# Optimization experiments

Hardware: AMD Instinct MI355X
Metric: run time of the kernel (lower is better)

The kernel has to match this reference:

```python
import jax, jax.numpy as jnp
import numpy as np

C_S = 128
C_T = 128
C_OUT = 128


def _proj(x, W, b):
    # 1x1x1 Conv3d == per-voxel linear over channel dim. x: [B, Cin, T, H, W]
    return jnp.einsum('oc,bcthw->bothw', W, x) + b[None, :, None, None, None]


def setup_inputs() -> dict:
    key = jax.random.key(0)
    ks = jax.random.split(key, 12)
    B, T, H, W = 4, 4, 32, 32
    spatial_features = jax.random.normal(ks[0], (B, T, C_S, H, W), dtype=jnp.float32)
    temporal_features = jax.random.normal(ks[1], (B, C_T, T, H, W), dtype=jnp.float32)
    def w(k, o, i):
        return jax.random.normal(k, (o, i), dtype=jnp.float32) * (i ** -0.5)
    return {
        'spatial_features': spatial_features,
        'temporal_features': temporal_features,
        'Wq': w(ks[2], C_OUT, C_S), 'bq': jnp.zeros((C_OUT,), jnp.float32),
        'Wk': w(ks[3], C_OUT, C_T), 'bk': jnp.zeros((C_OUT,), jnp.float32),
        'Wv': w(ks[4], C_OUT, C_T), 'bv': jnp.zeros((C_OUT,), jnp.float32),
        'Wo': w(ks[5], C_OUT, C_OUT), 'bo': jnp.zeros((C_OUT,), jnp.float32),
    }


def reference(spatial_features, temporal_features, Wq, bq, Wk, bk, Wv, bv, Wo, bo):
    B, T, C_s, H, W = spatial_features.shape
    N = T * H * W
    scale = C_OUT ** -0.5
    # permute(0,2,1,3,4): [B, T, C_s, H, W] -> [B, C_s, T, H, W]
    x_s = jnp.transpose(spatial_features, (0, 2, 1, 3, 4))
    q = _proj(x_s, Wq, bq)                 # [B, C_out, T, H, W]
    k = _proj(temporal_features, Wk, bk)   # [B, C_out, T, H, W]
    v = _proj(temporal_features, Wv, bv)   # [B, C_out, T, H, W]
    Q = q.reshape(B, C_OUT, N).transpose(0, 2, 1)  # [B, N, C]
    K = k.reshape(B, C_OUT, N)                     # [B, C, N]
    V = v.reshape(B, C_OUT, N).transpose(0, 2, 1)  # [B, N, C]
    attn = jax.nn.softmax(jnp.einsum('bnc,bcm->bnm', Q, K) * scale, axis=2)  # [B, N, N]
    out = jnp.einsum('bnm,bmc->bnc', attn, V)      # [B, N, C]
    out = out.transpose(0, 2, 1).reshape(B, C_OUT, T, H, W)
    return _proj(out, Wo, bo)
```

## Files before the change

### kernel.cpp

```cpp
#include <hip/hip_runtime.h>
#include <cstddef>

#define NDIM 4096
#define SCALE 0.08838834764831843f
#define SOFT_BIAS 8.0f

typedef _Float16 h8 __attribute__((ext_vector_type(8)));
typedef _Float16 h4 __attribute__((ext_vector_type(4)));
typedef _Float16 h2 __attribute__((ext_vector_type(2)));
typedef float    f4 __attribute__((ext_vector_type(4)));

__global__ __launch_bounds__(256) void prep_w_kernel(
    const float* __restrict__ Wq, const float* __restrict__ Wk,
    const float* __restrict__ Wv, const float* __restrict__ Wo,
    _Float16* __restrict__ Wh)
{
    const int idx = (blockIdx.x * 256 + threadIdx.x) * 8;
    const int sel = idx >> 14;
    const float* src = sel == 0 ? Wq : sel == 1 ? Wk : sel == 2 ? Wv : Wo;
    const int off = idx & 16383;
    const float4 a = *(const float4*)(src + off);
    const float4 c = *(const float4*)(src + off + 4);
    h8 r;
    r[0]=(_Float16)a.x; r[1]=(_Float16)a.y; r[2]=(_Float16)a.z; r[3]=(_Float16)a.w;
    r[4]=(_Float16)c.x; r[5]=(_Float16)c.y; r[6]=(_Float16)c.z; r[7]=(_Float16)c.w;
    *(h8*)(Wh + idx) = r;
}

__global__ __launch_bounds__(256, 1) void proj_qkv_kernel(
    const float* __restrict__ spatial, const float* __restrict__ temporal,
    const _Float16* __restrict__ Wh,
    const float* __restrict__ bq, const float* __restrict__ bk,
    const float* __restrict__ bv,
    _Float16* __restrict__ Qh, _Float16* __restrict__ Kh, _Float16* __restrict__ Vt)
{
    __shared__ __align__(16) _Float16 Xs[64 * 152];
    __shared__ __align__(16) _Float16 Xt[64 * 152];
    const int tid = threadIdx.x;
    const int n0  = blockIdx.x * 64;
    const int b   = blockIdx.y;
    const int t   = n0 >> 10, hw0 = n0 & 1023;

    #pragma unroll
    for (int i = 0; i < 8; ++i) {
        const int ii = tid + 256 * i;
        const int c = ii >> 4, j = ii & 15;
        const float4 v = *(const float4*)(spatial + (((size_t)(b * 4 + t) * 128 + c) << 10)
                                          + hw0 + 4 * j);
        Xs[(4 * j + 0) * 152 + c] = (_Float16)v.x;
        Xs[(4 * j + 1) * 152 + c] = (_Float16)v.y;
        Xs[(4 * j + 2) * 152 + c] = (_Float16)v.z;
        Xs[(4 * j + 3) * 152 + c] = (_Float16)v.w;
    }
    #pragma unroll
    for (int i = 0; i < 8; ++i) {
        const int ii = tid + 256 * i;
        const int c = ii >> 4, j = ii & 15;
        const float4 v = *(const float4*)(temporal + (((size_t)(b * 128 + c)) << 12)
                                          + n0 + 4 * j);
        Xt[(4 * j + 0) * 152 + c] = (_Float16)v.x;
        Xt[(4 * j + 1) * 152 + c] = (_Float16)v.y;
        Xt[(4 * j + 2) * 152 + c] = (_Float16)v.z;
        Xt[(4 * j + 3) * 152 + c] = (_Float16)v.w;
    }
    __syncthreads();

    const int w = tid >> 6, n16 = tid & 15, q4 = (tid >> 4) & 3;
    const _Float16* __restrict__ Whq = Wh;
    const _Float16* __restrict__ Whk = Wh + 16384;
    const _Float16* __restrict__ Whv = Wh + 32768;

    h8 xs_f[4], xt_f[4];
    #pragma unroll
    for (int ks = 0; ks < 4; ++ks) {
        xs_f[ks] = *(const h8*)&Xs[(16 * w + n16) * 152 + 32 * ks + 8 * q4];
        xt_f[ks] = *(const h8*)&Xt[(16 * w + n16) * 152 + 32 * ks + 8 * q4];
    }

    {
        f4 acc[8];
        #pragma unroll
        for (int ot = 0; ot < 8; ++ot) acc[ot] = (f4)0.0f;
        #pragma unroll
        for (int ot = 0; ot < 8; ++ot)
            #pragma unroll
            for (int ks = 0; ks < 4; ++ks) {
                const h8 af = *(const h8*)(Whq + (16 * ot + n16) * 128 + 32 * ks + 8 * q4);
                acc[ot] = __builtin_amdgcn_mfma_f32_16x16x32_f16(af, xs_f[ks], acc[ot], 0, 0, 0);
            }
        #pragma unroll
        for (int ot = 0; ot < 8; ++ot) {
            const float4 bb = *(const float4*)&bq[16 * ot + 4 * q4];
            h4 r;
            r[0]=(_Float16)(acc[ot][0]+bb.x); r[1]=(_Float16)(acc[ot][1]+bb.y);
            r[2]=(_Float16)(acc[ot][2]+bb.z); r[3]=(_Float16)(acc[ot][3]+bb.w);
            *(h4*)(Qh + ((size_t)b * NDIM + n0 + 16 * w + n16) * 128 + 16 * ot + 4 * q4) = r;
        }
    }
    {
        f4 acc[8];
        #pragma unroll
        for (int ot = 0; ot < 8; ++ot) acc[ot] = (f4)0.0f;
        #pragma unroll
        for (int ot = 0; ot < 8; ++ot)
            #pragma unroll
            for (int ks = 0; ks < 4; ++ks) {
                const h8 af = *(const h8*)(Whk + (16 * ot + n16) * 128 + 32 * ks + 8 * q4);
                acc[ot] = __builtin_amdgcn_mfma_f32_16x16x32_f16(af, xt_f[ks], acc[ot], 0, 0, 0);
            }
        #pragma unroll
        for (int ot = 0; ot < 8; ++ot) {
            const float4 bb = *(const float4*)&bk[16 * ot + 4 * q4];
            h4 r;
            r[0]=(_Float16)(acc[ot][0]+bb.x); r[1]=(_Float16)(acc[ot][1]+bb.y);
            r[2]=(_Float16)(acc[ot][2]+bb.z); r[3]=(_Float16)(acc[ot][3]+bb.w);
            *(h4*)(Kh + ((size_t)b * NDIM + n0 + 16 * w + n16) * 128 + 16 * ot + 4 * q4) = r;
        }
    }
    {
        f4 acc[8];
        #pragma unroll
        for (int ct = 0; ct < 8; ++ct) acc[ct] = (f4)0.0f;
        #pragma unroll
        for (int ct = 0; ct < 8; ++ct)
            #pragma unroll
            for (int ks = 0; ks < 4; ++ks) {
                const h8 bf = *(const h8*)(Whv + (16 * ct + n16) * 128 + 32 * ks + 8 * q4);
                acc[ct] = __builtin_amdgcn_mfma_f32_16x16x32_f16(xt_f[ks], bf, acc[ct], 0, 0, 0);
            }
        #pragma unroll
        for (int ct = 0; ct < 8; ++ct) {
            const float bb = bv[16 * ct + n16];
            h4 r;
            r[0]=(_Float16)(acc[ct][0]+bb); r[1]=(_Float16)(acc[ct][1]+bb);
            r[2]=(_Float16)(acc[ct][2]+bb); r[3]=(_Float16)(acc[ct][3]+bb);
            *(h4*)(Vt + ((size_t)(b * 128 + 16 * ct + n16) << 12) + n0 + 16 * w + 4 * q4) = r;
        }
    }
}

__global__ __launch_bounds__(256, 2) void attn_kernel(
    const _Float16* __restrict__ Qh, const _Float16* __restrict__ Kh,
    const _Float16* __restrict__ Vt, _Float16* __restrict__ Opart,
    float* __restrict__ lpart)
{
    __shared__ __align__(16) _Float16 sh[14592];
    __shared__ float lred[2][2][32];
    _Float16* __restrict__ Kt = sh;
    _Float16* __restrict__ Vl = sh + 4352;
    _Float16* __restrict__ Pa = sh + 9472;

    const int tid  = threadIdx.x;
    const int w    = tid >> 6, lane = tid & 63;
    const int g    = w >> 1,  p    = w & 1;
    const int n16  = lane & 15, q4 = lane >> 4;
    const int b    = blockIdx.z, hf = blockIdx.y;
    const int n0   = blockIdx.x * 128;
    const int mb   = hf * 1024;

    _Float16* __restrict__ Pg = Pa + g * (64 * 40);

    h8 qf[4][4];
    {
        const _Float16* Qb = Qh + ((size_t)b * NDIM + n0 + 64 * g + n16) * 128;
        #pragma unroll
        for (int qs = 0; qs < 4; ++qs)
            #pragma unroll
            for (int ks = 0; ks < 4; ++ks)
                qf[qs][ks] = *(const h8*)(Qb + (size_t)(16 * qs) * 128 + 32 * ks + 8 * q4);
    }

    const int km  = tid >> 4, kc8 = (tid & 15) * 8;
    const int vc  = tid >> 2, vm8 = (tid & 3) * 8;
    const _Float16* kp = Kh + ((size_t)b * NDIM + mb + km) * 128 + kc8;
    const _Float16* vp = Vt + (((size_t)(b * 128 + vc)) << 12) + mb + vm8;
    int4 kreg0 = *(const int4*)kp;
    int4 kreg1 = *(const int4*)(kp + (size_t)16 * 128);
    int4 vreg0 = *(const int4*)vp;
    int4 vreg1 = *(const int4*)(vp + ((size_t)64 << 12));

    f4 oacc[4][4];
    #pragma unroll
    for (int i = 0; i < 4; ++i)
        #pragma unroll
        for (int j = 0; j < 4; ++j) oacc[i][j] = (f4)0.0f;
    float lsum[4] = {0.0f, 0.0f, 0.0f, 0.0f};

    for (int it = 0; it < 32; ++it) {
        __syncthreads();
        *(int4*)&Kt[km * 136 + kc8]        = kreg0;
        *(int4*)&Kt[(16 + km) * 136 + kc8] = kreg1;
        *(int4*)&Vl[vc * 40 + vm8]         = vreg0;
        *(int4*)&Vl[(64 + vc) * 40 + vm8]  = vreg1;
        __syncthreads();

        if (it < 31) {
            kp += 32 * 128; vp += 32;
            kreg0 = *(const int4*)kp;
            kreg1 = *(const int4*)(kp + (size_t)16 * 128);
            vreg0 = *(const int4*)vp;
            vreg1 = *(const int4*)(vp + ((size_t)64 << 12));
        }

        f4 sacc[4];
        #pragma unroll
        for (int qs = 0; qs < 4; ++qs) sacc[qs] = (f4)0.0f;
        #pragma unroll
        for (int ks = 0; ks < 4; ++ks) {
            const h8 kf = *(const h8*)&Kt[(16 * p + n16) * 136 + 32 * ks + 8 * q4];
            #pragma unroll
            for (int qs = 0; qs < 4; ++qs)
                sacc[qs] = __builtin_amdgcn_mfma_f32_16x16x32_f16(kf, qf[qs][ks], sacc[qs], 0, 0, 0);
        }

        #pragma unroll
        for (int qs = 0; qs < 4; ++qs) {
            h4 pk;
            #pragma unroll
            for (int r = 0; r < 4; ++r) {
                const float e = __expf(fmaf(sacc[qs][r], SCALE, -SOFT_BIAS));
                lsum[qs] += e;
                pk[r] = (_Float16)e;
            }
            *(h4*)&Pg[(16 * qs + n16) * 40 + 16 * p + 4 * q4] = pk;
        }
        __syncthreads();

        h8 pf[4], vf[4];
        #pragma unroll
        for (int qs = 0; qs < 4; ++qs)
            pf[qs] = *(const h8*)&Pg[(16 * qs + n16) * 40 + 8 * q4];
        #pragma unroll
        for (int ct = 0; ct < 4; ++ct)
            vf[ct] = *(const h8*)&Vl[(64 * p + 16 * ct + n16) * 40 + 8 * q4];
        #pragma unroll
        for (int qs = 0; qs < 4; ++qs)
            #pragma unroll
            for (int ct = 0; ct < 4; ++ct)
                oacc[qs][ct] = __builtin_amdgcn_mfma_f32_16x16x32_f16(pf[qs], vf[ct], oacc[qs][ct], 0, 0, 0);
    }

    #pragma unroll
    for (int qs = 0; qs < 4; ++qs) {
        lsum[qs] += __shfl_xor(lsum[qs], 16, 64);
        lsum[qs] += __shfl_xor(lsum[qs], 32, 64);
    }
    __syncthreads();
    if (q4 == 0) {
        #pragma unroll
        for (int qs = 0; qs < 4; ++qs) lred[g][p][0] = lred[g][p][0];
        #pragma unroll
        for (int qs = 0; qs < 2; ++qs) {
            lred[g][p][16 * qs + n16]      = lsum[qs];
        }
    }
    __syncthreads();
    if (q4 == 0) {
        float* lb = lpart + (size_t)(hf * 4 + b) * NDIM + n0 + 64 * g;
        if (p == 0) {
            #pragma unroll
            for (int qs = 0; qs < 2; ++qs)
                lb[16 * qs + n16] = lred[g][0][16 * qs + n16] + lred[g][1][16 * qs + n16];
        }
    }
    __syncthreads();
    if (q4 == 0) {
        #pragma unroll
        for (int qs = 2; qs < 4; ++qs)
            lred[g][p][16 * (qs - 2) + n16] = lsum[qs];
    }
    __syncthreads();
    if (q4 == 0 && p == 0) {
        float* lb = lpart + (size_t)(hf * 4 + b) * NDIM + n0 + 64 * g + 32;
        #pragma unroll
        for (int qs = 0; qs < 2; ++qs)
            lb[16 * qs + n16] = lred[g][0][16 * qs + n16] + lred[g][1][16 * qs + n16];
    }

    for (int g2 = 0; g2 < 2; ++g2) {
        __syncthreads();
        if (g == g2) {
            #pragma unroll
            for (int qs = 0; qs < 4; ++qs)
                #pragma unroll
                for (int ct = 0; ct < 4; ++ct)
                    #pragma unroll
                    for (int r = 0; r < 4; ++r)
                        sh[(16 * qs + 4 * q4 + r) * 136 + 64 * p + 16 * ct + n16] =
                            (_Float16)oacc[qs][ct][r];
        }
        __syncthreads();
        const size_t ob = ((size_t)(hf * 4 + b) * NDIM + n0 + 64 * g2) * 128;
        #pragma unroll
        for (int i = 0; i < 4; ++i) {
            const int ii  = tid + 256 * i;
            const int row = ii >> 4, c8 = (ii & 15) * 8;
            *(int4*)(Opart + ob + (size_t)row * 128 + c8) = *(const int4*)&sh[row * 136 + c8];
        }
    }
}

__global__ __launch_bounds__(256, 1) void proj_final_kernel(
    const _Float16* __restrict__ Opart, const float* __restrict__ lpart,
    const _Float16* __restrict__ Who, const float* __restrict__ bo,
    float* __restrict__ out)
{
    __shared__ __align__(16) _Float16 Xl[64 * 136];
    __shared__ __align__(16) float Ofin[128 * 68];
    const int tid = threadIdx.x;
    const int n0  = blockIdx.x * 64;
    const int b   = blockIdx.y;

    #pragma unroll
    for (int i = 0; i < 4; ++i) {
        const int ii  = tid + 256 * i;
        const int row = ii >> 4, c8 = (ii & 15) * 8;
        float vals[8] = {0,0,0,0,0,0,0,0};
        float l = 0.0f;
        #pragma unroll
        for (int hf = 0; hf < 4; ++hf) {
            const size_t base = ((size_t)(hf * 4 + b) * NDIM + n0 + row) * 128 + c8;
            const h8 o = *(const h8*)(Opart + base);
            #pragma unroll
            for (int j = 0; j < 8; ++j) vals[j] += (float)o[j];
            l += lpart[(size_t)(hf * 4 + b) * NDIM + n0 + row];
        }
        const float rinv = 1.0f / l;
        h8 r;
        #pragma unroll
        for (int j = 0; j < 8; ++j) r[j] = (_Float16)(vals[j] * rinv);
        *(h8*)&Xl[row * 136 + c8] = r;
    }
    __syncthreads();

    const int w = tid >> 6, n16 = tid & 15, q4 = (tid >> 4) & 3;

    h8 xf[4];
    #pragma unroll
    for (int ks = 0; ks < 4; ++ks)
        xf[ks] = *(const h8*)&Xl[(16 * w + n16) * 136 + 32 * ks + 8 * q4];

    f4 acc[8];
    #pragma unroll
    for (int ot = 0; ot < 8; ++ot) acc[ot] = (f4)0.0f;

    #pragma unroll
    for (int ot = 0; ot < 8; ++ot)
        #pragma unroll
        for (int ks = 0; ks < 4; ++ks) {
            const h8 af = *(const h8*)(Who + (16 * ot + n16) * 128 + 32 * ks + 8 * q4);
            acc[ot] = __builtin_amdgcn_mfma_f32_16x16x32_f16(af, xf[ks], acc[ot], 0, 0, 0);
        }

    #pragma unroll
    for (int ot = 0; ot < 8; ++ot) {
        const float4 bb = *(const float4*)&bo[16 * ot + 4 * q4];
        const float bias[4] = {bb.x, bb.y, bb.z, bb.w};
        #pragma unroll
        for (int r = 0; r < 4; ++r)
            Ofin[(16 * ot + 4 * q4 + r) * 68 + 16 * w + n16] = acc[ot][r] + bias[r];
    }
    __syncthreads();
    #pragma unroll
    for (int i = 0; i < 8; ++i) {
        const int ii  = tid + 256 * i;
        const int row = ii >> 4, j = ii & 15;
        *(float4*)(out + (((size_t)(b * 128 + row)) << 12) + n0 + 4 * j) =
            *(const float4*)&Ofin[row * 68 + 4 * j];
    }
}

extern "C" void kernel_launch(void* const* d_in, const int* in_sizes, int n_in,
                              void* d_out, int out_size, void* d_ws, size_t ws_size,
                              hipStream_t stream)
{
    const float* spatial  = (const float*)d_in[0];
    const float* temporal = (const float*)d_in[1];
    const float* Wq = (const float*)d_in[2];
    const float* bq = (const float*)d_in[3];
    const float* Wk = (const float*)d_in[4];
    const float* bk = (const float*)d_in[5];
    const float* Wv = (const float*)d_in[6];
    const float* bv = (const float*)d_in[7];
    const float* Wo = (const float*)d_in[8];
    const float* bo = (const float*)d_in[9];

    char* ws = (char*)d_ws;
    _Float16* Qh    = (_Float16*)(ws);
    _Float16* Kh    = (_Float16*)(ws + (4u  << 20));
    _Float16* Vt    = (_Float16*)(ws + (8u  << 20));
    _Float16* Opart = (_Float16*)(ws + (12u << 20));
    float*    lpart = (float*)   (ws + (28u << 20));
    _Float16* Wh    = (_Float16*)(ws + (28u << 20) + (256u << 10));

    prep_w_kernel<<<32, 256, 0, stream>>>(Wq, Wk, Wv, Wo, Wh);
    proj_qkv_kernel<<<dim3(64, 4), 256, 0, stream>>>(spatial, temporal, Wh,
                                                     bq, bk, bv, Qh, Kh, Vt);
    attn_kernel<<<dim3(32, 4, 4), 256, 0, stream>>>(Qh, Kh, Vt, Opart, lpart);
    proj_final_kernel<<<dim3(64, 4), 256, 0, stream>>>(Opart, lpart, Wh + 49152, bo,
                                                       (float*)d_out);
}
```

Measured before the change: 164.0 us.

## Drop weight prep kernel, split QKV projection grid, widen attention KV tiles

Removes the separate fp32-to-fp16 weight conversion kernel and converts weights on the fly inside the projection kernels. The QKV projection kernel is split by projection and by smaller 32-row tiles, and the output projection also uses 32-row tiles, both to launch more blocks and improve occupancy. The attention kernel processes 64 keys per iteration instead of 32, halving barrier count per key. It writes per-wave partial row sums straight to global memory instead of reducing them through shared memory, and the final kernel sums eight partials. This trades extra redundant weight loads and conversions, and more LDS in attention, for fewer launches and syncs.

```diff
diff --git a/kernel.cpp b/kernel.cpp
--- a/kernel.cpp
+++ b/kernel.cpp
@@ -10,132 +10,118 @@
 typedef _Float16 h2 __attribute__((ext_vector_type(2)));
 typedef float    f4 __attribute__((ext_vector_type(4)));
 
-__global__ __launch_bounds__(256) void prep_w_kernel(
+__device__ __forceinline__ h8 cvt_w_frag(const float* wp) {
+    const float4 u0 = *(const float4*)wp;
+    const float4 u1 = *(const float4*)(wp + 4);
+    h8 f;
+    f[0]=(_Float16)u0.x; f[1]=(_Float16)u0.y; f[2]=(_Float16)u0.z; f[3]=(_Float16)u0.w;
+    f[4]=(_Float16)u1.x; f[5]=(_Float16)u1.y; f[6]=(_Float16)u1.z; f[7]=(_Float16)u1.w;
+    return f;
+}
+
+__global__ __launch_bounds__(256, 2) void proj_qkv_kernel(
+    const float* __restrict__ spatial, const float* __restrict__ temporal,
     const float* __restrict__ Wq, const float* __restrict__ Wk,
-    const float* __restrict__ Wv, const float* __restrict__ Wo,
-    _Float16* __restrict__ Wh)
-{
-    const int idx = (blockIdx.x * 256 + threadIdx.x) * 8;
-    const int sel = idx >> 14;
-    const float* src = sel == 0 ? Wq : sel == 1 ? Wk : sel == 2 ? Wv : Wo;
-    const int off = idx & 16383;
-    const float4 a = *(const float4*)(src + off);
-    const float4 c = *(const float4*)(src + off + 4);
-    h8 r;
-    r[0]=(_Float16)a.x; r[1]=(_Float16)a.y; r[2]=(_Float16)a.z; r[3]=(_Float16)a.w;
-    r[4]=(_Float16)c.x; r[5]=(_Float16)c.y; r[6]=(_Float16)c.z; r[7]=(_Float16)c.w;
-    *(h8*)(Wh + idx) = r;
-}
-
-__global__ __launch_bounds__(256, 1) void proj_qkv_kernel(
-    const float* __restrict__ spatial, const float* __restrict__ temporal,
-    const _Float16* __restrict__ Wh,
+    const float* __restrict__ Wv,
     const float* __restrict__ bq, const float* __restrict__ bk,
     const float* __restrict__ bv,
     _Float16* __restrict__ Qh, _Float16* __restrict__ Kh, _Float16* __restrict__ Vt)
 {
-    __shared__ __align__(16) _Float16 Xs[64 * 152];
-    __shared__ __align__(16) _Float16 Xt[64 * 152];
+    __shared__ __align__(16) _Float16 Xl[32 * 136];
     const int tid = threadIdx.x;
-    const int n0  = blockIdx.x * 64;
+    const int n0  = blockIdx.x * 32;
     const int b   = blockIdx.y;
-    const int t   = n0 >> 10, hw0 = n0 & 1023;
-
-    #pragma unroll
-    for (int i = 0; i < 8; ++i) {
-        const int ii = tid + 256 * i;
-        const int c = ii >> 4, j = ii & 15;
-        const float4 v = *(const float4*)(spatial + (((size_t)(b * 4 + t) * 128 + c) << 10)
-                                          + hw0 + 4 * j);
-        Xs[(4 * j + 0) * 152 + c] = (_Float16)v.x;
-        Xs[(4 * j + 1) * 152 + c] = (_Float16)v.y;
-        Xs[(4 * j + 2) * 152 + c] = (_Float16)v.z;
-        Xs[(4 * j + 3) * 152 + c] = (_Float16)v.w;
-    }
-    #pragma unroll
-    for (int i = 0; i < 8; ++i) {
-        const int ii = tid + 256 * i;
-        const int c = ii >> 4, j = ii & 15;
-        const float4 v = *(const float4*)(temporal + (((size_t)(b * 128 + c)) << 12)
-                                          + n0 + 4 * j);
-        Xt[(4 * j + 0) * 152 + c] = (_Float16)v.x;
-        Xt[(4 * j + 1) * 152 + c] = (_Float16)v.y;
-        Xt[(4 * j + 2) * 152 + c] = (_Float16)v.z;
-        Xt[(4 * j + 3) * 152 + c] = (_Float16)v.w;
+    const int p   = blockIdx.z;
+
+    const float* __restrict__ W    = (p == 0) ? Wq : (p == 1) ? Wk : Wv;
+    const float* __restrict__ bias = (p == 0) ? bq : (p == 1) ? bk : bv;
+
+    {
+        const float* src; size_t rs;
+        if (p == 0) { const int t = n0 >> 10, hw0 = n0 & 1023;
+            src = spatial + (((size_t)(b * 4 + t) * 128) << 10) + hw0; rs = 1024; }
+        else { src = temporal + ((size_t)(b * 128) << 12) + n0; rs = 4096; }
+        #pragma unroll
+        for (int i = 0; i < 2; ++i) {
+            const int ii = tid + 256 * i;
+            const int c2 = ii >> 3, j = ii & 7;
+            const float4 v0 = *(const float4*)(src + (size_t)(2 * c2) * rs + 4 * j);
+            const float4 v1 = *(const float4*)(src + (size_t)(2 * c2 + 1) * rs + 4 * j);
+            const float a0[4] = {v0.x, v0.y, v0.z, v0.w};
+            const float a1[4] = {v1.x, v1.y, v1.z, v1.w};
+            #pragma unroll
+            for (int u = 0; u < 4; ++u) {
+                h2 pk; pk[0] = (_Float16)a0[u]; pk[1] = (_Float16)a1[u];
+                *(h2*)&Xl[(4 * j + u) * 136 + 2 * c2] = pk;
+            }
+        }
     }
     __syncthreads();
 
     const int w = tid >> 6, n16 = tid & 15, q4 = (tid >> 4) & 3;
-    const _Float16* __restrict__ Whq = Wh;
-    const _Float16* __restrict__ Whk = Wh + 16384;
-    const _Float16* __restrict__ Whv = Wh + 32768;
-
-    h8 xs_f[4], xt_f[4];
-    #pragma unroll
-    for (int ks = 0; ks < 4; ++ks) {
-        xs_f[ks] = *(const h8*)&Xs[(16 * w + n16) * 152 + 32 * ks + 8 * q4];
-        xt_f[ks] = *(const h8*)&Xt[(16 * w + n16) * 152 + 32 * ks + 8 * q4];
-    }
-
-    {
-        f4 acc[8];
-        #pragma unroll
-        for (int ot = 0; ot < 8; ++ot) acc[ot] = (f4)0.0f;
-        #pragma unroll
-        for (int ot = 0; ot < 8; ++ot)
-            #pragma unroll
-            for (int ks = 0; ks < 4; ++ks) {
-                const h8 af = *(const h8*)(Whq + (16 * ot + n16) * 128 + 32 * ks + 8 * q4);
-                acc[ot] = __builtin_amdgcn_mfma_f32_16x16x32_f16(af, xs_f[ks], acc[ot], 0, 0, 0);
-            }
-        #pragma unroll
-        for (int ot = 0; ot < 8; ++ot) {
-            const float4 bb = *(const float4*)&bq[16 * ot + 4 * q4];
-            h4 r;
-            r[0]=(_Float16)(acc[ot][0]+bb.x); r[1]=(_Float16)(acc[ot][1]+bb.y);
-            r[2]=(_Float16)(acc[ot][2]+bb.z); r[3]=(_Float16)(acc[ot][3]+bb.w);
-            *(h4*)(Qh + ((size_t)b * NDIM + n0 + 16 * w + n16) * 128 + 16 * ot + 4 * q4) = r;
-        }
-    }
-    {
-        f4 acc[8];
-        #pragma unroll
-        for (int ot = 0; ot < 8; ++ot) acc[ot] = (f4)0.0f;
-        #pragma unroll
-        for (int ot = 0; ot < 8; ++ot)
-            #pragma unroll
-            for (int ks = 0; ks < 4; ++ks) {
-                const h8 af = *(const h8*)(Whk + (16 * ot + n16) * 128 + 32 * ks + 8 * q4);
-                acc[ot] = __builtin_amdgcn_mfma_f32_16x16x32_f16(af, xt_f[ks], acc[ot], 0, 0, 0);
-            }
-        #pragma unroll
-        for (int ot = 0; ot < 8; ++ot) {
-            const float4 bb = *(const float4*)&bk[16 * ot + 4 * q4];
-            h4 r;
-            r[0]=(_Float16)(acc[ot][0]+bb.x); r[1]=(_Float16)(acc[ot][1]+bb.y);
-            r[2]=(_Float16)(acc[ot][2]+bb.z); r[3]=(_Float16)(acc[ot][3]+bb.w);
-            *(h4*)(Kh + ((size_t)b * NDIM + n0 + 16 * w + n16) * 128 + 16 * ot + 4 * q4) = r;
-        }
-    }
-    {
-        f4 acc[8];
-        #pragma unroll
-        for (int ct = 0; ct < 8; ++ct) acc[ct] = (f4)0.0f;
-        #pragma unroll
-        for (int ct = 0; ct < 8; ++ct)
-            #pragma unroll
-            for (int ks = 0; ks < 4; ++ks) {
-                const h8 bf = *(const h8*)(Whv + (16 * ct + n16) * 128 + 32 * ks + 8 * q4);
-                acc[ct] = __builtin_amdgcn_mfma_f32_16x16x32_f16(xt_f[ks], bf, acc[ct], 0, 0, 0);
-            }
-        #pragma unroll
-        for (int ct = 0; ct < 8; ++ct) {
-            const float bb = bv[16 * ct + n16];
-            h4 r;
-            r[0]=(_Float16)(acc[ct][0]+bb); r[1]=(_Float16)(acc[ct][1]+bb);
-            r[2]=(_Float16)(acc[ct][2]+bb); r[3]=(_Float16)(acc[ct][3]+bb);
-            *(h4*)(Vt + ((size_t)(b * 128 + 16 * ct + n16) << 12) + n0 + 16 * w + 4 * q4) = r;
-        }
+
+    h8 wf[2][4];
+    #pragma unroll
+    for (int otl = 0; otl < 2; ++otl)
+        #pragma unroll
+        for (int ks = 0; ks < 4; ++ks)
+            wf[otl][ks] = cvt_w_frag(W + (size_t)(16 * (2 * w + otl) + n16) * 128
+                                       + 32 * ks + 8 * q4);
+    h8 xf[2][4];
+    #pragma unroll
+    for (int ns = 0; ns < 2; ++ns)
+        #pragma unroll
+        for (int ks = 0; ks < 4; ++ks)
+            xf[ns][ks] = *(const h8*)&Xl[(16 * ns + n16) * 136 + 32 * ks + 8 * q4];
+
+    if (p < 2) {
+        f4 acc[2][2];
+        #pragma unroll
+        for (int i = 0; i < 2; ++i) { acc[i][0] = (f4)0.0f; acc[i][1] = (f4)0.0f; }
+        #pragma unroll
+        for (int otl = 0; otl < 2; ++otl)
+            #pragma unroll
+            for (int ns = 0; ns < 2; ++ns)
+                #pragma unroll
+                for (int ks = 0; ks < 4; ++ks)
+                    acc[otl][ns] = __builtin_amdgcn_mfma_f32_16x16x32_f16(
+                        wf[otl][ks], xf[ns][ks], acc[otl][ns], 0, 0, 0);
+        _Float16* __restrict__ dst = (p == 0) ? Qh : Kh;
+        #pragma unroll
+        for (int otl = 0; otl < 2; ++otl) {
+            const float4 bb = *(const float4*)&bias[16 * (2 * w + otl) + 4 * q4];
+            #pragma unroll
+            for (int ns = 0; ns < 2; ++ns) {
+                h4 r;
+                r[0]=(_Float16)(acc[otl][ns][0]+bb.x); r[1]=(_Float16)(acc[otl][ns][1]+bb.y);
+                r[2]=(_Float16)(acc[otl][ns][2]+bb.z); r[3]=(_Float16)(acc[otl][ns][3]+bb.w);
+                *(h4*)(dst + ((size_t)b * NDIM + n0 + 16 * ns + n16) * 128
+                           + 16 * (2 * w + otl) + 4 * q4) = r;
+            }
+        }
+    } else {
+        f4 acc[2][2];
+        #pragma unroll
+        for (int i = 0; i < 2; ++i) { acc[i][0] = (f4)0.0f; acc[i][1] = (f4)0.0f; }
+        #pragma unroll
+        for (int ns = 0; ns < 2; ++ns)
+            #pragma unroll
+            for (int otl = 0; otl < 2; ++otl)
+                #pragma unroll
+                for (int ks = 0; ks < 4; ++ks)
+                    acc[ns][otl] = __builtin_amdgcn_mfma_f32_16x16x32_f16(
+                        xf[ns][ks], wf[otl][ks], acc[ns][otl], 0, 0, 0);
+        #pragma unroll
+        for (int ns = 0; ns < 2; ++ns)
+            #pragma unroll
+            for (int otl = 0; otl < 2; ++otl) {
+                const float bb = bias[16 * (2 * w + otl) + n16];
+                h4 r;
+                r[0]=(_Float16)(acc[ns][otl][0]+bb); r[1]=(_Float16)(acc[ns][otl][1]+bb);
+                r[2]=(_Float16)(acc[ns][otl][2]+bb); r[3]=(_Float16)(acc[ns][otl][3]+bb);
+                *(h4*)(Vt + ((size_t)(b * 128 + 16 * (2 * w + otl) + n16) << 12)
+                          + n0 + 16 * ns + 4 * q4) = r;
+            }
     }
 }
 
@@ -144,11 +130,10 @@
     const _Float16* __restrict__ Vt, _Float16* __restrict__ Opart,
     float* __restrict__ lpart)
 {
-    __shared__ __align__(16) _Float16 sh[14592];
-    __shared__ float lred[2][2][32];
+    __shared__ __align__(16) _Float16 sh[27136];
     _Float16* __restrict__ Kt = sh;
-    _Float16* __restrict__ Vl = sh + 4352;
-    _Float16* __restrict__ Pa = sh + 9472;
+    _Float16* __restrict__ Vl = sh + 8704;
+    _Float16* __restrict__ Pa = sh + 17920;
 
     const int tid  = threadIdx.x;
     const int w    = tid >> 6, lane = tid & 63;
@@ -158,7 +143,7 @@
     const int n0   = blockIdx.x * 128;
     const int mb   = hf * 1024;
 
-    _Float16* __restrict__ Pg = Pa + g * (64 * 40);
+    _Float16* __restrict__ Pg = Pa + g * 4608;
 
     h8 qf[4][4];
     {
@@ -170,14 +155,16 @@
                 qf[qs][ks] = *(const h8*)(Qb + (size_t)(16 * qs) * 128 + 32 * ks + 8 * q4);
     }
 
-    const int km  = tid >> 4, kc8 = (tid & 15) * 8;
-    const int vc  = tid >> 2, vm8 = (tid & 3) * 8;
+    const int km  = tid >> 2, kc8 = (tid & 3) * 32;
+    const int vc  = tid >> 1, vm8 = (tid & 1) * 32;
     const _Float16* kp = Kh + ((size_t)b * NDIM + mb + km) * 128 + kc8;
     const _Float16* vp = Vt + (((size_t)(b * 128 + vc)) << 12) + mb + vm8;
-    int4 kreg0 = *(const int4*)kp;
-    int4 kreg1 = *(const int4*)(kp + (size_t)16 * 128);
-    int4 vreg0 = *(const int4*)vp;
-    int4 vreg1 = *(const int4*)(vp + ((size_t)64 << 12));
+    int4 kreg[4], vreg[4];
+    #pragma unroll
+    for (int j = 0; j < 4; ++j) {
+        kreg[j] = *(const int4*)(kp + 8 * j);
+        vreg[j] = *(const int4*)(vp + 8 * j);
+    }
 
     f4 oacc[4][4];
     #pragma unroll
@@ -186,58 +173,67 @@
         for (int j = 0; j < 4; ++j) oacc[i][j] = (f4)0.0f;
     float lsum[4] = {0.0f, 0.0f, 0.0f, 0.0f};
 
-    for (int it = 0; it < 32; ++it) {
+    for (int it = 0; it < 16; ++it) {
         __syncthreads();
-        *(int4*)&Kt[km * 136 + kc8]        = kreg0;
-        *(int4*)&Kt[(16 + km) * 136 + kc8] = kreg1;
-        *(int4*)&Vl[vc * 40 + vm8]         = vreg0;
-        *(int4*)&Vl[(64 + vc) * 40 + vm8]  = vreg1;
+        #pragma unroll
+        for (int j = 0; j < 4; ++j) {
+            *(int4*)&Kt[km * 136 + kc8 + 8 * j] = kreg[j];
+            *(int4*)&Vl[vc * 72  + vm8 + 8 * j] = vreg[j];
+        }
         __syncthreads();
 
-        if (it < 31) {
-            kp += 32 * 128; vp += 32;
-            kreg0 = *(const int4*)kp;
-            kreg1 = *(const int4*)(kp + (size_t)16 * 128);
-            vreg0 = *(const int4*)vp;
-            vreg1 = *(const int4*)(vp + ((size_t)64 << 12));
-        }
-
-        f4 sacc[4];
-        #pragma unroll
-        for (int qs = 0; qs < 4; ++qs) sacc[qs] = (f4)0.0f;
-        #pragma unroll
-        for (int ks = 0; ks < 4; ++ks) {
-            const h8 kf = *(const h8*)&Kt[(16 * p + n16) * 136 + 32 * ks + 8 * q4];
+        if (it < 15) {
+            kp += 64 * 128; vp += 64;
+            #pragma unroll
+            for (int j = 0; j < 4; ++j) {
+                kreg[j] = *(const int4*)(kp + 8 * j);
+                vreg[j] = *(const int4*)(vp + 8 * j);
+            }
+        }
+
+        #pragma unroll
+        for (int mt2 = 0; mt2 < 2; ++mt2) {
+            f4 s[4];
+            #pragma unroll
+            for (int qs = 0; qs < 4; ++qs) s[qs] = (f4)0.0f;
+            #pragma unroll
+            for (int ks = 0; ks < 4; ++ks) {
+                const h8 kf = *(const h8*)&Kt[(16 * (2 * p + mt2) + n16) * 136
+                                              + 32 * ks + 8 * q4];
+                #pragma unroll
+                for (int qs = 0; qs < 4; ++qs)
+                    s[qs] = __builtin_amdgcn_mfma_f32_16x16x32_f16(kf, qf[qs][ks], s[qs], 0, 0, 0);
+            }
+            #pragma unroll
+            for (int qs = 0; qs < 4; ++qs) {
+                h4 pk;
+                #pragma unroll
+                for (int r = 0; r < 4; ++r) {
+                    const float e = __expf(fmaf(s[qs][r], SCALE, -SOFT_BIAS));
+                    lsum[qs] += e;
+                    pk[r] = (_Float16)e;
+                }
+                *(h4*)&Pg[(16 * qs + n16) * 72 + 32 * p + 16 * mt2 + 4 * q4] = pk;
+            }
+        }
+        __syncthreads();
+
+        #pragma unroll
+        for (int kk = 0; kk < 2; ++kk) {
+            h8 pf[4], vf[4];
             #pragma unroll
             for (int qs = 0; qs < 4; ++qs)
-                sacc[qs] = __builtin_amdgcn_mfma_f32_16x16x32_f16(kf, qf[qs][ks], sacc[qs], 0, 0, 0);
-        }
-
-        #pragma unroll
-        for (int qs = 0; qs < 4; ++qs) {
-            h4 pk;
-            #pragma unroll
-            for (int r = 0; r < 4; ++r) {
-                const float e = __expf(fmaf(sacc[qs][r], SCALE, -SOFT_BIAS));
-                lsum[qs] += e;
-                pk[r] = (_Float16)e;
-            }
-            *(h4*)&Pg[(16 * qs + n16) * 40 + 16 * p + 4 * q4] = pk;
-        }
-        __syncthreads();
-
-        h8 pf[4], vf[4];
-        #pragma unroll
-        for (int qs = 0; qs < 4; ++qs)
-            pf[qs] = *(const h8*)&Pg[(16 * qs + n16) * 40 + 8 * q4];
-        #pragma unroll
-        for (int ct = 0; ct < 4; ++ct)
-            vf[ct] = *(const h8*)&Vl[(64 * p + 16 * ct + n16) * 40 + 8 * q4];
-        #pragma unroll
-        for (int qs = 0; qs < 4; ++qs)
+                pf[qs] = *(const h8*)&Pg[(16 * qs + n16) * 72 + 32 * kk + 8 * q4];
             #pragma unroll
             for (int ct = 0; ct < 4; ++ct)
-                oacc[qs][ct] = __builtin_amdgcn_mfma_f32_16x16x32_f16(pf[qs], vf[ct], oacc[qs][ct], 0, 0, 0);
+                vf[ct] = *(const h8*)&Vl[(64 * p + 16 * ct + n16) * 72 + 32 * kk + 8 * q4];
+            #pragma unroll
+            for (int qs = 0; qs < 4; ++qs)
+                #pragma unroll
+                for (int ct = 0; ct < 4; ++ct)
+                    oacc[qs][ct] = __builtin_amdgcn_mfma_f32_16x16x32_f16(
+                        pf[qs], vf[ct], oacc[qs][ct], 0, 0, 0);
+        }
     }
 
     #pragma unroll
@@ -245,128 +241,123 @@
         lsum[qs] += __shfl_xor(lsum[qs], 16, 64);
         lsum[qs] += __shfl_xor(lsum[qs], 32, 64);
     }
-    __syncthreads();
     if (q4 == 0) {
-        #pragma unroll
-        for (int qs = 0; qs < 4; ++qs) lred[g][p][0] = lred[g][p][0];
-        #pragma unroll
-        for (int qs = 0; qs < 2; ++qs) {
-            lred[g][p][16 * qs + n16]      = lsum[qs];
-        }
-    }
-    __syncthreads();
-    if (q4 == 0) {
-        float* lb = lpart + (size_t)(hf * 4 + b) * NDIM + n0 + 64 * g;
-        if (p == 0) {
-            #pragma unroll
-            for (int qs = 0; qs < 2; ++qs)
-                lb[16 * qs + n16] = lred[g][0][16 * qs + n16] + lred[g][1][16 * qs + n16];
-        }
-    }
-    __syncthreads();
-    if (q4 == 0) {
-        #pragma unroll
-        for (int qs = 2; qs < 4; ++qs)
-            lred[g][p][16 * (qs - 2) + n16] = lsum[qs];
-    }
-    __syncthreads();
-    if (q4 == 0 && p == 0) {
-        float* lb = lpart + (size_t)(hf * 4 + b) * NDIM + n0 + 64 * g + 32;
-        #pragma unroll
-        for (int qs = 0; qs < 2; ++qs)
-            lb[16 * qs + n16] = lred[g][0][16 * qs + n16] + lred[g][1][16 * qs + n16];
-    }
-
-    for (int g2 = 0; g2 < 2; ++g2) {
-        __syncthreads();
-        if (g == g2) {
-            #pragma unroll
-            for (int qs = 0; qs < 4; ++qs)
-                #pragma unroll
-                for (int ct = 0; ct < 4; ++ct)
-                    #pragma unroll
-                    for (int r = 0; r < 4; ++r)
-                        sh[(16 * qs + 4 * q4 + r) * 136 + 64 * p + 16 * ct + n16] =
-                            (_Float16)oacc[qs][ct][r];
-        }
-        __syncthreads();
-        const size_t ob = ((size_t)(hf * 4 + b) * NDIM + n0 + 64 * g2) * 128;
-        #pragma unroll
-        for (int i = 0; i < 4; ++i) {
-            const int ii  = tid + 256 * i;
-            const int row = ii >> 4, c8 = (ii & 15) * 8;
-            *(int4*)(Opart + ob + (size_t)row * 128 + c8) = *(const int4*)&sh[row * 136 + c8];
-        }
-    }
-}
-
-__global__ __launch_bounds__(256, 1) void proj_final_kernel(
+        float* lb = lpart + ((size_t)((hf * 2 + p) * 4 + b)) * NDIM + n0 + 64 * g;
+        #pragma unroll
+        for (int qs = 0; qs < 4; ++qs) lb[16 * qs + n16] = lsum[qs];
+    }
+
+    __syncthreads();
+    #pragma unroll
+    for (int qs = 0; qs < 4; ++qs)
+        #pragma unroll
+        for (int ct = 0; ct < 4; ++ct)
+            #pragma unroll
+            for (int r = 0; r < 4; ++r)
+                sh[(64 * g + 16 * qs + 4 * q4 + r) * 136 + 64 * p + 16 * ct + n16] =
+                    (_Float16)oacc[qs][ct][r];
+    __syncthreads();
+    const size_t ob = ((size_t)(hf * 4 + b) * NDIM + n0) * 128;
+    #pragma unroll
+    for (int i = 0; i < 8; ++i) {
+        const int ii  = tid + 256 * i;
+        const int row = ii >> 4, c8 = (ii & 15) * 8;
+        *(int4*)(Opart + ob + (size_t)row * 128 + c8) = *(const int4*)&sh[row * 136 + c8];
+    }
+}
+
+__global__ __launch_bounds__(256, 2) void proj_final_kernel(
     const _Float16* __restrict__ Opart, const float* __restrict__ lpart,
-    const _Float16* __restrict__ Who, const float* __restrict__ bo,
+    const float* __restrict__ Wo, const float* __restrict__ bo,
     float* __restrict__ out)
 {
-    __shared__ __align__(16) _Float16 Xl[64 * 136];
-    __shared__ __align__(16) float Ofin[128 * 68];
+    __shared__ __align__(16) _Float16 Xl[32 * 136];
+    __shared__ float lrow[32];
+    __shared__ __align__(16) float Ofin[128 * 36];
     const int tid = threadIdx.x;
-    const int n0  = blockIdx.x * 64;
+    const int n0  = blockIdx.x * 32;
     const int b   = blockIdx.y;
 
+    if (tid < 32) {
+        float l = 0.0f;
+        #pragma unroll
+        for (int h8i = 0; h8i < 8; ++h8i)
+            l += lpart[((size_t)(h8i * 4 + b)) * NDIM + n0 + tid];
+        lrow[tid] = 1.0f / l;
+    }
+    float vals[2][8];
+    int rows[2], c8s[2];
+    #pragma unroll
+    for (int i = 0; i < 2; ++i) {
+        const int ii = tid + 256 * i;
+        rows[i] = ii >> 4; c8s[i] = (ii & 15) * 8;
+        #pragma unroll
+        for (int j = 0; j < 8; ++j) vals[i][j] = 0.0f;
+        #pragma unroll
+        for (int hf = 0; hf < 4; ++hf) {
+            const h8 o = *(const h8*)(Opart + ((size_t)(hf * 4 + b) * NDIM + n0 + rows[i]) * 128
+                                      + c8s[i]);
+            #pragma unroll
+            for (int j = 0; j < 8; ++j) vals[i][j] += (float)o[j];
+        }
+    }
+    __syncthreads();
+    #pragma unroll
+    for (int i = 0; i < 2; ++i) {
+        const float linv = lrow[rows[i]];
+        h8 r;
+        #pragma unroll
+        for (int j = 0; j < 8; ++j) r[j] = (_Float16)(vals[i][j] * linv);
+        *(h8*)&Xl[rows[i] * 136 + c8s[i]] = r;
+    }
+    __syncthreads();
+
+    const int w = tid >> 6, n16 = tid & 15, q4 = (tid >> 4) & 3;
+
+    h8 wf[2][4];
+    #pragma unroll
+    for (int otl = 0; otl < 2; ++otl)
+        #pragma unroll
+        for (int ks = 0; ks < 4; ++ks)
+            wf[otl][ks] = cvt_w_frag(Wo + (size_t)(16 * (2 * w + otl) + n16) * 128
+                                        + 32 * ks + 8 * q4);
+    h8 xf[2][4];
+    #pragma unroll
+    for (int ns = 0; ns < 2; ++ns)
+        #pragma unroll
+        for (int ks = 0; ks < 4; ++ks)
+            xf[ns][ks] = *(const h8*)&Xl[(16 * ns + n16) * 136 + 32 * ks + 8 * q4];
+
+    f4 acc[2][2];
+    #pragma unroll
+    for (int i = 0; i < 2; ++i) { acc[i][0] = (f4)0.0f; acc[i][1] = (f4)0.0f; }
+    #pragma unroll
+    for (int otl = 0; otl < 2; ++otl)
+        #pragma unroll
+        for (int ns = 0; ns < 2; ++ns)
+            #pragma unroll
+            for (int ks = 0; ks < 4; ++ks)
+                acc[otl][ns] = __builtin_amdgcn_mfma_f32_16x16x32_f16(
+                    wf[otl][ks], xf[ns][ks], acc[otl][ns], 0, 0, 0);
+
+    #pragma unroll
+    for (int otl = 0; otl < 2; ++otl) {
+        const float4 bb = *(const float4*)&bo[16 * (2 * w + otl) + 4 * q4];
+        const float bias[4] = {bb.x, bb.y, bb.z, bb.w};
+        #pragma unroll
+        for (int ns = 0; ns < 2; ++ns)
+            #pragma unroll
+            for (int r = 0; r < 4; ++r)
+                Ofin[(16 * (2 * w + otl) + 4 * q4 + r) * 36 + 16 * ns + n16] =
+                    acc[otl][ns][r] + bias[r];
+    }
+    __syncthreads();
     #pragma unroll
     for (int i = 0; i < 4; ++i) {
         const int ii  = tid + 256 * i;
-        const int row = ii >> 4, c8 = (ii & 15) * 8;
-        float vals[8] = {0,0,0,0,0,0,0,0};
-        float l = 0.0f;
-        #pragma unroll
-        for (int hf = 0; hf < 4; ++hf) {
-            const size_t base = ((size_t)(hf * 4 + b) * NDIM + n0 + row) * 128 + c8;
-            const h8 o = *(const h8*)(Opart + base);
-            #pragma unroll
-            for (int j = 0; j < 8; ++j) vals[j] += (float)o[j];
-            l += lpart[(size_t)(hf * 4 + b) * NDIM + n0 + row];
-        }
-        const float rinv = 1.0f / l;
-        h8 r;
-        #pragma unroll
-        for (int j = 0; j < 8; ++j) r[j] = (_Float16)(vals[j] * rinv);
-        *(h8*)&Xl[row * 136 + c8] = r;
-    }
-    __syncthreads();
-
-    const int w = tid >> 6, n16 = tid & 15, q4 = (tid >> 4) & 3;
-
-    h8 xf[4];
-    #pragma unroll
-    for (int ks = 0; ks < 4; ++ks)
-        xf[ks] = *(const h8*)&Xl[(16 * w + n16) * 136 + 32 * ks + 8 * q4];
-
-    f4 acc[8];
-    #pragma unroll
-    for (int ot = 0; ot < 8; ++ot) acc[ot] = (f4)0.0f;
-
-    #pragma unroll
-    for (int ot = 0; ot < 8; ++ot)
-        #pragma unroll
-        for (int ks = 0; ks < 4; ++ks) {
-            const h8 af = *(const h8*)(Who + (16 * ot + n16) * 128 + 32 * ks + 8 * q4);
-            acc[ot] = __builtin_amdgcn_mfma_f32_16x16x32_f16(af, xf[ks], acc[ot], 0, 0, 0);
-        }
-
-    #pragma unroll
-    for (int ot = 0; ot < 8; ++ot) {
-        const float4 bb = *(const float4*)&bo[16 * ot + 4 * q4];
-        const float bias[4] = {bb.x, bb.y, bb.z, bb.w};
-        #pragma unroll
-        for (int r = 0; r < 4; ++r)
-            Ofin[(16 * ot + 4 * q4 + r) * 68 + 16 * w + n16] = acc[ot][r] + bias[r];
-    }
-    __syncthreads();
-    #pragma unroll
-    for (int i = 0; i < 8; ++i) {
-        const int ii  = tid + 256 * i;
-        const int row = ii >> 4, j = ii & 15;
+        const int row = ii >> 3, j = ii & 7;
         *(float4*)(out + (((size_t)(b * 128 + row)) << 12) + n0 + 4 * j) =
-            *(const float4*)&Ofin[row * 68 + 4 * j];
+            *(const float4*)&Ofin[row * 36 + 4 * j];
     }
 }
 
@@ -391,12 +382,10 @@
     _Float16* Vt    = (_Float16*)(ws + (8u  << 20));
     _Float16* Opart = (_Float16*)(ws + (12u << 20));
     float*    lpart = (float*)   (ws + (28u << 20));
-    _Float16* Wh    = (_Float16*)(ws + (28u << 20) + (256u << 10));
-
-    prep_w_kernel<<<32, 256, 0, stream>>>(Wq, Wk, Wv, Wo, Wh);
-    proj_qkv_kernel<<<dim3(64, 4), 256, 0, stream>>>(spatial, temporal, Wh,
-                                                     bq, bk, bv, Qh, Kh, Vt);
+
+    proj_qkv_kernel<<<dim3(128, 4, 3), 256, 0, stream>>>(
+        spatial, temporal, Wq, Wk, Wv, bq, bk, bv, Qh, Kh, Vt);
     attn_kernel<<<dim3(32, 4, 4), 256, 0, stream>>>(Qh, Kh, Vt, Opart, lpart);
-    proj_final_kernel<<<dim3(64, 4), 256, 0, stream>>>(Opart, lpart, Wh + 49152, bo,
-                                                       (float*)d_out);
-}
+    proj_final_kernel<<<dim3(128, 4), 256, 0, stream>>>(Opart, lpart, Wo, bo,
+                                                        (float*)d_out);
+}
```

Measured after the change: 195.1 us. +19.0%, slower.
